# Performance work log

Measured on AMD Instinct MI355X. Metric: run time of the kernel, lower is better.

Reference implementation:

```python
import jax, jax.numpy as jnp
import numpy as np

KH, KW = 3, 3
STRIDE = (1, 1)
PAD = (1, 1)
DIL = (1, 1)

def _unfold(x, kh, kw, stride, padding, dilation):
    # Faithful torch.nn.functional.unfold: output (B, C*kh*kw, L) with
    # feature ordering channel-slowest, then kh, then kw.
    B, C, H, W = x.shape
    h_out = (H + 2 * padding[0] - dilation[0] * (kh - 1) - 1) // stride[0] + 1
    w_out = (W + 2 * padding[1] - dilation[1] * (kw - 1) - 1) // stride[1] + 1
    xp = jnp.pad(x, ((0, 0), (0, 0), (padding[0], padding[0]), (padding[1], padding[1])))
    rows = []
    for i in range(kh):  # small fixed kernel loop (9 slices), not a data-dim loop
        for j in range(kw):
            r0 = i * dilation[0]
            c0 = j * dilation[1]
            patch = xp[:, :, r0:r0 + h_out * stride[0]:stride[0],
                             c0:c0 + w_out * stride[1]:stride[1]]  # (B,C,h_out,w_out)
            rows.append(patch)
    # stack -> (B, C, kh*kw, h_out, w_out); reorder so feature dim = C*kh*kw
    p = jnp.stack(rows, axis=2)
    p = p.reshape(B, C * kh * kw, h_out * w_out)
    return p, h_out, w_out

def transform_transposed_unfolded_input(inp_unf):
    # Default hook: identity (as in the base class).
    return inp_unf

def reference(x, weight, bias):
    B = x.shape[0]
    O = weight.shape[0]
    inp_unf, h_out, w_out = _unfold(x, KH, KW, STRIDE, PAD, DIL)   # (B, C*k*k, L)
    inp_t = jnp.swapaxes(inp_unf, 1, 2)                            # (B, L, C*k*k)
    inp_t = transform_transposed_unfolded_input(inp_t)
    w2d = weight.reshape(O, -1)                                    # (O, C*k*k)
    out_unf = jnp.einsum('blk,ok->bol', inp_t, w2d)                # (B, O, L)
    out = out_unf.reshape(B, O, h_out, w_out)
    out = out + bias.reshape(1, O, 1, 1)
    return out

def setup_inputs() -> dict:
    key = jax.random.key(0)
    k1, k2, k3 = jax.random.split(key, 3)
    x = jax.random.normal(k1, (32, 128, 56, 56), dtype=jnp.float32)
    fan_in = 128 * KH * KW
    weight = jax.random.normal(k2, (256, 128, KH, KW), dtype=jnp.float32) / np.sqrt(fan_in)
    bias = jax.random.normal(k3, (256,), dtype=jnp.float32) * 0.01
    return {"x": x, "weight": weight, "bias": bias}
```

## Files before the change

### kernel.cpp

```cpp
#include <hip/hip_runtime.h>
#include <hip/hip_bf16.h>
#include <cstdint>

typedef float f32x4 __attribute__((ext_vector_type(4)));
typedef short bf16x8 __attribute__((ext_vector_type(8)));

#define CIN   128
#define WIMG  56
#define HWSZ  3136
#define OCH   256
#define HP    58
#define WP    58
#define NT    18

__global__ void zero_border(__hip_bfloat16* __restrict__ xb) {
    int idx = blockIdx.x * 256 + threadIdx.x;
    int c8  = idx & 15;
    int t   = idx >> 4;
    int b   = t / 228;
    int pos = t - b * 228;
    int h, w;
    if (pos < 58)       { h = 0;             w = pos; }
    else if (pos < 116) { h = 57;            w = pos - 58; }
    else if (pos < 172) { h = pos - 116 + 1; w = 0; }
    else                { h = pos - 172 + 1; w = 57; }
    uint4 z = {0, 0, 0, 0};
    *(uint4*)((char*)xb + (((size_t)(b * HP + h) * WP + w) * CIN + c8 * 8) * 2) = z;
}

__global__ void cast_transpose_x(const float* __restrict__ x,
                                 __hip_bfloat16* __restrict__ xb) {
    __shared__ float tile[32][33];
    const int hw0 = blockIdx.x * 32;
    const int c0  = blockIdx.y * 32;
    const int b   = blockIdx.z;
    const int tx  = threadIdx.x;
    const int ty  = threadIdx.y;

    const float* src = x + ((size_t)(b * CIN + c0) * HWSZ) + hw0;
#pragma unroll
    for (int k = 0; k < 4; ++k) {
        int c = ty + k * 8;
        tile[c][tx] = src[(size_t)c * HWSZ + tx];
    }
    __syncthreads();
#pragma unroll
    for (int k = 0; k < 4; ++k) {
        int hwl = ty + k * 8;
        int hw = hw0 + hwl;
        int h = hw / WIMG;
        int w = hw - h * WIMG;
        size_t dst = (((size_t)b * HP + (h + 1)) * WP + (w + 1)) * CIN + c0 + tx;
        xb[dst] = __float2bfloat16(tile[tx][hwl]);
    }
}

__global__ void prep_w(const float* __restrict__ wsrc,
                       __hip_bfloat16* __restrict__ wb) {
    int idx = blockIdx.x * 256 + threadIdx.x;
    int c    = idx & 127;
    int rest = idx >> 7;
    int o    = rest & 255;
    int ij   = rest >> 8;
    wb[idx] = __float2bfloat16(wsrc[((size_t)o * CIN + c) * 9 + ij]);
}

__device__ __forceinline__ void gload16(const void* g, void* l) {
    __builtin_amdgcn_global_load_lds(
        (const __attribute__((address_space(1))) unsigned*)g,
        (__attribute__((address_space(3))) unsigned*)l,
        16, 0, 0);
}

__global__ __launch_bounds__(512, 2)
void conv_gemm(const __hip_bfloat16* __restrict__ xb,
               const __hip_bfloat16* __restrict__ wb,
               const float* __restrict__ bias,
               float* __restrict__ out) {
    extern __shared__ __attribute__((aligned(16))) char smem[];

    const int tid = threadIdx.x;
    const int wv  = tid >> 6;
    const int ln  = tid & 63;

    int bid = blockIdx.x;
    bid = (bid & 7) * 49 + (bid >> 3);
    const int m0 = bid * 256;

    const int srow = tid >> 3;
    const int cs   = tid & 7;
    const int colsrc = ((cs * 16) ^ ((srow & 7) << 4)) >> 1;
    int aOff[4], bOff[4];
#pragma unroll
    for (int q = 0; q < 4; ++q) {
        int row = q * 64 + srow;
        int p  = m0 + row;
        int b  = p / HWSZ;
        int hw = p - b * HWSZ;
        int h  = hw / WIMG;
        int w  = hw - h * WIMG;
        aOff[q] = ((b * HP + h) * WP + w) * CIN + colsrc;
        bOff[q] = row * CIN + colsrc;
    }
    const int ldsd = tid * 16;

#define SA(buf,q,offA_) gload16(xb + aOff[q] + (offA_), smem + (buf)*65536 + (q)*8192 + ldsd)
#define SB(buf,q,offB_) gload16(wb + bOff[q] + (offB_), smem + (buf)*65536 + 32768 + (q)*8192 + ldsd)

    const int wm  = wv >> 2;
    const int wn  = wv & 3;
    const int fr  = ln & 15;
    const int kby = (ln >> 4) * 16;
    const int swz = (ln & 7) << 4;

    f32x4 acc[8][4] = {};
    bf16x8 af[4][2], bq0[2][2], bq1[2][2];

#define READ_A(base, mh) do {                                                 \
    _Pragma("unroll") for (int mi = 0; mi < 4; ++mi)                          \
    _Pragma("unroll") for (int kk = 0; kk < 2; ++kk)                          \
        af[mi][kk] = *(const bf16x8*)((base) +                                \
            (wm*128 + (mh)*64 + mi*16 + fr)*128 + ((kk*64 + kby) ^ swz));     \
} while (0)

#define READ_B(base, nh, dst) do {                                            \
    _Pragma("unroll") for (int ni = 0; ni < 2; ++ni)                          \
    _Pragma("unroll") for (int kk = 0; kk < 2; ++kk)                          \
        dst[ni][kk] = *(const bf16x8*)((base) + 32768 +                       \
            (wn*64 + (nh)*32 + ni*16 + fr)*128 + ((kk*64 + kby) ^ swz));      \
} while (0)

#define MQ(mh, nh, B) do {                                                    \
    _Pragma("unroll") for (int kk = 0; kk < 2; ++kk)                          \
    _Pragma("unroll") for (int mi = 0; mi < 4; ++mi)                          \
    _Pragma("unroll") for (int ni = 0; ni < 2; ++ni)                          \
        acc[(mh)*4+mi][(nh)*2+ni] = __builtin_amdgcn_mfma_f32_16x16x32_bf16(  \
            af[mi][kk], B[ni][kk], acc[(mh)*4+mi][(nh)*2+ni], 0, 0, 0);       \
} while (0)

    SA(0,0,0); SA(0,1,0); SA(0,2,0); SA(0,3,0);
    SB(0,0,0); SB(0,1,0); SB(0,2,0); SB(0,3,0);
    asm volatile("s_waitcnt vmcnt(0)" ::: "memory");
    __builtin_amdgcn_s_barrier();

#pragma unroll 2
    for (int t = 0; t < NT; ++t) {
        const int cur = t & 1;
        const char* base = smem + cur * 65536;
        const int  nx = cur ^ 1;
        const bool pf = (t + 1 < NT);
        const int s   = t + 1;
        const int ij  = s >> 1;
        const int ck0 = (s & 1) << 6;
        const int ii  = ij / 3;
        const int jj  = ij - ii * 3;
        const int offA = (ii * WP + jj) * CIN + ck0;
        const int offB = ij * (OCH * CIN) + ck0;

        if (pf) { SA(nx,0,offA); SA(nx,1,offA); SA(nx,2,offA); }
        READ_A(base, 0);
        READ_B(base, 0, bq0);
        __builtin_amdgcn_s_barrier();
        asm volatile("s_waitcnt lgkmcnt(0)" ::: "memory");
        __builtin_amdgcn_s_setprio(1);
        MQ(0, 0, bq0);
        __builtin_amdgcn_s_setprio(0);
        __builtin_amdgcn_s_barrier();

        if (pf) { SA(nx,3,offA); SB(nx,0,offB); SB(nx,1,offB); }
        READ_B(base, 1, bq1);
        __builtin_amdgcn_s_barrier();
        asm volatile("s_waitcnt lgkmcnt(0)" ::: "memory");
        __builtin_amdgcn_s_setprio(1);
        MQ(0, 1, bq1);
        __builtin_amdgcn_s_setprio(0);
        __builtin_amdgcn_s_barrier();

        if (pf) { SB(nx,2,offB); SB(nx,3,offB); }
        READ_A(base, 1);
        __builtin_amdgcn_s_barrier();
        asm volatile("s_waitcnt lgkmcnt(0)" ::: "memory");
        __builtin_amdgcn_s_setprio(1);
        MQ(1, 1, bq1);
        __builtin_amdgcn_s_setprio(0);
        __builtin_amdgcn_s_barrier();

        __builtin_amdgcn_s_setprio(1);
        MQ(1, 0, bq0);
        __builtin_amdgcn_s_setprio(0);
        asm volatile("s_waitcnt vmcnt(0)" ::: "memory");
        __builtin_amdgcn_s_barrier();
        __builtin_amdgcn_sched_barrier(0);
    }
#undef SA
#undef SB
#undef READ_A
#undef READ_B
#undef MQ

    const int laneR4 = (ln >> 4) * 4;
    float bn[4];
#pragma unroll
    for (int ni = 0; ni < 4; ++ni)
        bn[ni] = bias[wn * 64 + ni * 16 + fr];

#pragma unroll
    for (int mi = 0; mi < 8; ++mi) {
        int p0 = m0 + wm * 128 + mi * 16 + laneR4;
        int b  = p0 / HWSZ;
        int hw = p0 - b * HWSZ;
#pragma unroll
        for (int ni = 0; ni < 4; ++ni) {
            int n = wn * 64 + ni * 16 + fr;
            float4 v;
            v.x = acc[mi][ni][0] + bn[ni];
            v.y = acc[mi][ni][1] + bn[ni];
            v.z = acc[mi][ni][2] + bn[ni];
            v.w = acc[mi][ni][3] + bn[ni];
            *(float4*)(out + ((size_t)(b * OCH + n) * HWSZ + hw)) = v;
        }
    }
}

extern "C" void kernel_launch(void* const* d_in, const int* in_sizes, int n_in,
                              void* d_out, int out_size, void* d_ws, size_t ws_size,
                              hipStream_t stream) {
    const float* x    = (const float*)d_in[0];
    const float* w    = (const float*)d_in[1];
    const float* bias = (const float*)d_in[2];
    float* out = (float*)d_out;

    char* ws = (char*)d_ws;
    __hip_bfloat16* xbuf = (__hip_bfloat16*)ws;
    __hip_bfloat16* wbuf = (__hip_bfloat16*)(ws + 27557888);

    hipFuncSetAttribute(reinterpret_cast<const void*>(conv_gemm),
                        hipFuncAttributeMaxDynamicSharedMemorySize, 131072);

    zero_border<<<456, 256, 0, stream>>>(xbuf);
    cast_transpose_x<<<dim3(98, 4, 32), dim3(32, 8), 0, stream>>>(x, xbuf);
    prep_w<<<9 * 256 * 128 / 256, 256, 0, stream>>>(w, wbuf);
    conv_gemm<<<392, 512, 131072, stream>>>(xbuf, wbuf, bias, out);
}
```

Before: 105.1 us.

## Rework GEMM main loop into finer-grained async load pipeline with partial vmcnt waits

Replaces the 18-step double-buffered loop with a 9-iteration loop that handles both buffers explicitly. Global-to-LDS loads for the next stage are interleaved at a finer grain, and completion is tracked with partial vmcnt waits instead of draining everything each step. Loads for each buffer half are issued as soon as that region's data has been consumed, so they overlap more with MFMA work. This adds complexity and a correctness risk: a wrong vmcnt count or missing barrier could let a half-filled buffer be read.

```diff
diff --git a/kernel.cpp b/kernel.cpp
--- a/kernel.cpp
+++ b/kernel.cpp
@@ -138,65 +138,85 @@
             af[mi][kk], B[ni][kk], acc[(mh)*4+mi][(nh)*2+ni], 0, 0, 0);       \
 } while (0)
 
-    SA(0,0,0); SA(0,1,0); SA(0,2,0); SA(0,3,0);
-    SB(0,0,0); SB(0,1,0); SB(0,2,0); SB(0,3,0);
-    asm volatile("s_waitcnt vmcnt(0)" ::: "memory");
+#define PHASE_MFMA(mh, nh, B)                                                 \
+    __builtin_amdgcn_s_barrier();                                             \
+    asm volatile("s_waitcnt lgkmcnt(0)" ::: "memory");                        \
+    __builtin_amdgcn_s_setprio(1);                                            \
+    MQ(mh, nh, B);                                                            \
+    __builtin_amdgcn_s_setprio(0);                                            \
     __builtin_amdgcn_s_barrier();
 
-#pragma unroll 2
-    for (int t = 0; t < NT; ++t) {
-        const int cur = t & 1;
-        const char* base = smem + cur * 65536;
-        const int  nx = cur ^ 1;
-        const bool pf = (t + 1 < NT);
-        const int s   = t + 1;
-        const int ij  = s >> 1;
-        const int ck0 = (s & 1) << 6;
-        const int ii  = ij / 3;
-        const int jj  = ij - ii * 3;
-        const int offA = (ii * WP + jj) * CIN + ck0;
-        const int offB = ij * (OCH * CIN) + ck0;
-
-        if (pf) { SA(nx,0,offA); SA(nx,1,offA); SA(nx,2,offA); }
-        READ_A(base, 0);
-        READ_B(base, 0, bq0);
-        __builtin_amdgcn_s_barrier();
-        asm volatile("s_waitcnt lgkmcnt(0)" ::: "memory");
-        __builtin_amdgcn_s_setprio(1);
-        MQ(0, 0, bq0);
-        __builtin_amdgcn_s_setprio(0);
-        __builtin_amdgcn_s_barrier();
-
-        if (pf) { SA(nx,3,offA); SB(nx,0,offB); SB(nx,1,offB); }
-        READ_B(base, 1, bq1);
-        __builtin_amdgcn_s_barrier();
-        asm volatile("s_waitcnt lgkmcnt(0)" ::: "memory");
-        __builtin_amdgcn_s_setprio(1);
-        MQ(0, 1, bq1);
-        __builtin_amdgcn_s_setprio(0);
-        __builtin_amdgcn_s_barrier();
-
-        if (pf) { SB(nx,2,offB); SB(nx,3,offB); }
-        READ_A(base, 1);
-        __builtin_amdgcn_s_barrier();
-        asm volatile("s_waitcnt lgkmcnt(0)" ::: "memory");
-        __builtin_amdgcn_s_setprio(1);
-        MQ(1, 1, bq1);
-        __builtin_amdgcn_s_setprio(0);
-        __builtin_amdgcn_s_barrier();
-
+    const char* base0 = smem;
+    const char* base1 = smem + 65536;
+
+    SA(0,0,0); SA(0,2,0); SB(0,0,0); SB(0,1,0); SB(0,2,0); SB(0,3,0); SA(0,1,0); SA(0,3,0);
+    SA(1,0,64); SA(1,2,64);
+    asm volatile("s_waitcnt vmcnt(2)" ::: "memory");
+    __builtin_amdgcn_s_barrier();
+
+#pragma unroll 1
+    for (int i = 0; i < 9; ++i) {
+        const int iiA = i / 3,       jjA = i - 3 * iiA;
+        const int iiB = (i + 1) / 3, jjB = (i + 1) - 3 * iiB;
+        const int offA1 = (iiA * WP + jjA) * CIN + 64;
+        const int offB1 = i * (OCH * CIN) + 64;
+        const int offA2 = (iiB * WP + jjB) * CIN;
+        const int offB2 = (i + 1) * (OCH * CIN);
+        const int offA3 = offA2 + 64;
+        const bool pf = (i < 8);
+
+        SB(1,0,offB1); SB(1,1,offB1);
+        READ_A(base0, 0);
+        READ_B(base0, 0, bq0);
+        PHASE_MFMA(0, 0, bq0);
+
+        SB(1,2,offB1); SB(1,3,offB1);
+        READ_B(base0, 1, bq1);
+        PHASE_MFMA(0, 1, bq1);
+        asm volatile("s_waitcnt vmcnt(6)" ::: "memory");
+
+        SA(1,1,offA1); SA(1,3,offA1);
+        READ_A(base0, 1);
+        PHASE_MFMA(1, 1, bq1);
+
+        if (pf) { SA(0,0,offA2); SA(0,2,offA2); }
         __builtin_amdgcn_s_setprio(1);
         MQ(1, 0, bq0);
         __builtin_amdgcn_s_setprio(0);
-        asm volatile("s_waitcnt vmcnt(0)" ::: "memory");
+        if (pf) asm volatile("s_waitcnt vmcnt(4)" ::: "memory");
+        else    asm volatile("s_waitcnt vmcnt(2)" ::: "memory");
         __builtin_amdgcn_s_barrier();
-        __builtin_amdgcn_sched_barrier(0);
+
+        if (pf) { SB(0,0,offB2); SB(0,1,offB2); }
+        READ_A(base1, 0);
+        READ_B(base1, 0, bq0);
+        PHASE_MFMA(0, 0, bq0);
+
+        if (pf) { SB(0,2,offB2); SB(0,3,offB2); }
+        READ_B(base1, 1, bq1);
+        PHASE_MFMA(0, 1, bq1);
+        if (pf) asm volatile("s_waitcnt vmcnt(6)" ::: "memory");
+        else    asm volatile("s_waitcnt vmcnt(0)" ::: "memory");
+
+        if (pf) { SA(0,1,offA2); SA(0,3,offA2); }
+        READ_A(base1, 1);
+        PHASE_MFMA(1, 1, bq1);
+
+        if (pf) { SA(1,0,offA3); SA(1,2,offA3); }
+        __builtin_amdgcn_s_setprio(1);
+        MQ(1, 0, bq0);
+        __builtin_amdgcn_s_setprio(0);
+        if (pf) {
+            asm volatile("s_waitcnt vmcnt(4)" ::: "memory");
+            __builtin_amdgcn_s_barrier();
+        }
     }
 #undef SA
 #undef SB
 #undef READ_A
 #undef READ_B
 #undef MQ
+#undef PHASE_MFMA
 
     const int laneR4 = (ln >> 4) * 4;
     float bn[4];
```

Result: no change. 104.1 us (-0.9%).
